# Kernel tuning notes

Measured on AMD Instinct MI355X. Metric: run time of the kernel, lower is better.

Reference implementation:

```python
import jax, jax.numpy as jnp
import numpy as np

N, T, H, D = 8, 192, 1024, 128
P = 4            # t_patch_size (kernel = stride)
TP = T // P      # 48 patch tokens
E = 16384
HOUR, WDAY = 48, 7


def conv1d_patch(e, W, b):
    # e: [B, Cin, T]; W: [Cout, Cin, P]; kernel == stride == P (non-overlapping)
    B, Ci, Tt = e.shape
    e = e.reshape(B, Ci, Tt // P, P)
    return jnp.einsum('bctk,ock->bot', e, W) + b[None, :, None]  # [B, Cout, T']


def gcn_propagate(x, src, dst, coef):
    # x: [B, H, D] ; symmetric-normalized sparse A_hat @ x
    msg = x[:, src, :] * coef[None, :, None]
    return jnp.zeros_like(x).at[:, dst, :].add(msg)


def setup_inputs() -> dict:
    key = jax.random.key(0)
    ks = jax.random.split(key, 12)
    x = jax.random.normal(ks[0], (N, 1, T, H, 1), dtype=jnp.float32)
    x_mark = jax.random.randint(ks[1], (N, T, 2), 0, 7).astype(jnp.int64)
    edges = jax.random.randint(ks[2], (E, 2), 0, H).astype(jnp.int64)
    node_split = jnp.arange(H, dtype=jnp.int64).reshape(4, 256)
    s = 0.02
    params = {
        'hour_emb': jax.random.normal(ks[3], (HOUR, D), jnp.float32) * s,
        'weekday_emb': jax.random.normal(ks[4], (WDAY, D), jnp.float32) * s,
        'timeconv_w': jax.random.normal(ks[5], (D, D, P), jnp.float32) * s,
        'timeconv_b': jnp.zeros((D,), jnp.float32),
        'tconv_w': jax.random.normal(ks[6], (D, 1, P), jnp.float32) * s,
        'tconv_b': jnp.zeros((D,), jnp.float32),
        'W1': jax.random.normal(ks[7], (D, D), jnp.float32) * s,
        'b1': jnp.zeros((D,), jnp.float32),
        'W2': jax.random.normal(ks[8], (D, D), jnp.float32) * s,
        'b2': jnp.zeros((D,), jnp.float32),
    }
    return dict(x=x, x_mark=x_mark, edges=edges, node_split=node_split, **params)


def reference(x, x_mark, edges, node_split, hour_emb, weekday_emb,
              timeconv_w, timeconv_b, tconv_w, tconv_b, W1, b1, W2, b2):
    # ---- TimeEmb (TemporalEmbedding, hour_num='48') ----
    hour_x = hour_emb[x_mark[:, :, 1]]        # [N, T, D]
    wday_x = weekday_emb[x_mark[:, :, 0]]     # [N, T, D]
    time_emb = conv1d_patch((hour_x + wday_x).transpose(0, 2, 1),
                            timeconv_w, timeconv_b).transpose(0, 2, 1)  # [N, T', D]

    # ---- temporal value embedding ----
    xv = jnp.squeeze(x, (1, 4)).transpose(0, 2, 1).reshape(N * H, 1, T)  # [N*H,1,T]
    tv = conv1d_patch(xv, tconv_w, tconv_b)                 # [N*H, D, T']
    tv = tv.transpose(0, 2, 1).reshape(N, H, TP, D)         # [N, H, T', D]
    tv = tv.transpose(0, 2, 1, 3).reshape(N * TP, H, D)     # [N*T', H, D]

    # ---- 2-layer GCN with self-loops + symmetric normalization ----
    src = jnp.concatenate([edges[:, 0], jnp.arange(H)])
    dst = jnp.concatenate([edges[:, 1], jnp.arange(H)])
    deg = jnp.zeros((H,), tv.dtype).at[dst].add(1.0)
    coef = jax.lax.rsqrt(deg[src] * deg[dst])
    h = jax.nn.relu(gcn_propagate(tv, src, dst, coef) @ W1 + b1)
    token = gcn_propagate(h, src, dst, coef) @ W2 + b2      # [N*T', H, D]
    token = token.reshape(N, TP, H, D)

    # ---- per-group gather + mean pooling, interleaved per time step ----
    G = node_split.shape[0]
    grouped = token[:, :, node_split.reshape(-1), :].reshape(N, TP, G, -1, D)
    token = grouped.mean(axis=3).reshape(N, TP * G, D)      # [N, T'*G, D]

    time_rep = jnp.repeat(time_emb, G, axis=1)              # [N, T'*G, D]
    out = token + time_rep  # is_time == 1; eval mode -> no dropout
    return out, time_rep
```

## Files before the change

### kernel.cpp

```cpp
#include <hip/hip_runtime.h>
#include <hip/hip_bf16.h>

#define NN 8
#define TT 192
#define HH 1024
#define DD 128
#define TPP 48
#define EE 16384
#define NEDGE (EE + HH)
#define BB (NN * TPP)
#define NOUT (NN * TT * DD)

typedef short bf16x8 __attribute__((ext_vector_type(8)));
typedef float f32x4 __attribute__((ext_vector_type(4)));

__device__ __forceinline__ float bf2f(__hip_bfloat16 h) { return __bfloat162float(h); }
__device__ __forceinline__ float us2f(unsigned short u) {
  union { unsigned i; float f; } t;
  t.i = ((unsigned)u) << 16;
  return t.f;
}

__global__ __launch_bounds__(256) void k_setup(
    const int* __restrict__ edges, int* __restrict__ degE,
    const int* __restrict__ node_split, int* __restrict__ inv,
    const float* __restrict__ tw, float* __restrict__ twT,
    float* __restrict__ zbuf,
    const float* __restrict__ x, __hip_bfloat16* __restrict__ Xall) {
  __shared__ float tile[64][65];
  int tid = threadIdx.x, bid = blockIdx.x;
  int i = bid * 256 + tid;
  if (i < EE) atomicAdd(&degE[edges[2 * i + 1]], 1);
  if (i < HH) inv[node_split[i]] = i;
  if (i < 65536) twT[(i & 511) * DD + (i >> 9)] = tw[i];
  if (i < 6144) zbuf[i] = 0.f;

  int tt = bid % 24, st = bid / 24;
  int t0 = tt * 64, s0 = st * 64;
  int sl = tid & 63, r4 = tid >> 6;
#pragma unroll 4
  for (int ii = 0; ii < 16; ++ii) {
    int tl = ii * 4 + r4;
    tile[tl][sl] = x[(size_t)(t0 + tl) * HH + s0 + sl];
  }
  __syncthreads();
#pragma unroll 4
  for (int ii = 0; ii < 16; ++ii) {
    int sl2 = ii * 4 + r4;
    Xall[(size_t)(s0 + sl2) * 1536 + t0 + sl] = __float2bfloat16(tile[sl][sl2]);
  }
}

__global__ __launch_bounds__(1024) void k_scan(const int* __restrict__ degE,
                                               int* __restrict__ row_ptr,
                                               const float* __restrict__ tcw,
                                               const float* __restrict__ tcb,
                                               const float* __restrict__ W1,
                                               float* __restrict__ CW,
                                               const float* __restrict__ W2,
                                               __hip_bfloat16* __restrict__ w2sw) {
  int t = threadIdx.x, lane = t & 63, wid = t >> 6;
  int v = degE[t] + 1;
#pragma unroll
  for (int off = 1; off < 64; off <<= 1) {
    int u = __shfl_up(v, off, 64);
    if (lane >= off) v += u;
  }
  __shared__ int wsum[16];
  if (lane == 63) wsum[wid] = v;
  __syncthreads();
  if (t < 64) {
    int s = (lane < 16) ? wsum[lane] : 0;
#pragma unroll
    for (int off = 1; off < 16; off <<= 1) {
      int u = __shfl_up(s, off, 64);
      if (lane >= off) s += u;
    }
    if (lane < 16) wsum[lane] = s;
  }
  __syncthreads();
  int base = wid ? wsum[wid - 1] : 0;
  row_ptr[t + 1] = base + v;
  if (t == 0) row_ptr[0] = 0;

  if (t < 640) {
    int j = t >> 7, o = t & 127;
    float acc = 0.f;
    if (j < 4)
      for (int d = 0; d < DD; ++d) acc = fmaf(tcw[d * 4 + j], W1[d * DD + o], acc);
    else
      for (int d = 0; d < DD; ++d) acc = fmaf(tcb[d], W1[d * DD + o], acc);
    CW[j * DD + o] = acc;
  }
#pragma unroll 4
  for (int u = 0; u < 16; ++u) {
    int i = t * 16 + u;
    int n = i >> 7, k = i & 127;
    int dstb = n * 256 + (((k >> 3) ^ (n & 7)) * 16) + (k & 7) * 2;
    w2sw[dstb >> 1] = __float2bfloat16(W2[k * DD + n]);
  }
}

__global__ void k_scatter(const int* __restrict__ edges, const int* __restrict__ degE,
                          const int* __restrict__ row_ptr, const int* __restrict__ inv,
                          int* __restrict__ fill, int* __restrict__ csr_src,
                          float* __restrict__ csr_coef, float* __restrict__ csum,
                          float* __restrict__ QT) {
  int e = blockIdx.x * 256 + threadIdx.x;
  if (e >= NEDGE) return;
  int s, dt;
  if (e < EE) { s = edges[2 * e]; dt = edges[2 * e + 1]; }
  else        { s = dt = e - EE; }
  float ds = (float)(degE[s] + 1);
  float dd = (float)(degE[dt] + 1);
  float cf = rsqrtf(ds * dd);
  int pos = atomicAdd(&fill[dt], 1);
  int at = row_ptr[dt] + pos;
  csr_src[at] = s;
  csr_coef[at] = cf;
  atomicAdd(&csum[dt], cf);
  int g = inv[dt] >> 8;
  atomicAdd(&QT[s * 4 + g], cf * (1.0f / 256.0f));
}

__global__ __launch_bounds__(256) void k_spmm(
    const int* __restrict__ row_ptr, const int* __restrict__ csr_src,
    const float* __restrict__ csr_coef, const __hip_bfloat16* __restrict__ Xall,
    __hip_bfloat16* __restrict__ xbar,
    const int* __restrict__ xm, const float* __restrict__ hour_emb,
    const float* __restrict__ wday_emb, const float* __restrict__ twT,
    const float* __restrict__ tcb, float* __restrict__ out) {
  __shared__ float sL[2][512];
  int tid = threadIdx.x, bid = blockIdx.x;
  if (bid < HH) {
    int h = bid;
    int j0 = row_ptr[h], j1 = row_ptr[h + 1];
    float a0 = 0.f, a1 = 0.f, a2 = 0.f, a3 = 0.f, a4 = 0.f, a5 = 0.f;
    for (int j = j0; j < j1; ++j) {
      int s = csr_src[j];
      float cf = csr_coef[j];
      const unsigned* xr = (const unsigned*)(Xall + (size_t)s * 1536);
      unsigned u0 = xr[tid], u1 = xr[tid + 256], u2 = xr[tid + 512];
      union { unsigned i; float f; } lo, hi;
      lo.i = u0 << 16; hi.i = u0 & 0xffff0000u;
      a0 = fmaf(cf, lo.f, a0); a1 = fmaf(cf, hi.f, a1);
      lo.i = u1 << 16; hi.i = u1 & 0xffff0000u;
      a2 = fmaf(cf, lo.f, a2); a3 = fmaf(cf, hi.f, a3);
      lo.i = u2 << 16; hi.i = u2 & 0xffff0000u;
      a4 = fmaf(cf, lo.f, a4); a5 = fmaf(cf, hi.f, a5);
    }
    unsigned* xw = (unsigned*)(xbar + (size_t)h * 1536);
    union { __hip_bfloat16 h2[2]; unsigned u; } pk;
    pk.h2[0] = __float2bfloat16(a0); pk.h2[1] = __float2bfloat16(a1);
    xw[tid] = pk.u;
    pk.h2[0] = __float2bfloat16(a2); pk.h2[1] = __float2bfloat16(a3);
    xw[tid + 256] = pk.u;
    pk.h2[0] = __float2bfloat16(a4); pk.h2[1] = __float2bfloat16(a5);
    xw[tid + 512] = pk.u;
  } else {
    int bb = bid - HH;
    int half = tid >> 7, o = tid & 127;
    int b = bb * 2 + half;
    int n = b / TPP, tp = b % TPP;
    for (int k = 0; k < 4; ++k) {
      int t = tp * 4 + k;
      int wd = xm[(n * TT + t) * 2 + 0];
      int hr = xm[(n * TT + t) * 2 + 1];
      sL[half][o * 4 + k] = hour_emb[hr * DD + o] + wday_emb[wd * DD + o];
    }
    __syncthreads();
    float a0 = tcb[o], a1 = 0.f, a2 = 0.f, a3 = 0.f;
    for (int j = 0; j < 512; j += 4) {
      a0 = fmaf(sL[half][j + 0], twT[(j + 0) * DD + o], a0);
      a1 = fmaf(sL[half][j + 1], twT[(j + 1) * DD + o], a1);
      a2 = fmaf(sL[half][j + 2], twT[(j + 2) * DD + o], a2);
      a3 = fmaf(sL[half][j + 3], twT[(j + 3) * DD + o], a3);
    }
    float acc = (a0 + a1) + (a2 + a3);
    size_t base = (size_t)NOUT + ((size_t)n * TT + tp * 4) * DD + o;
    out[base] = acc;
    out[base + DD] = acc;
    out[base + 2 * DD] = acc;
    out[base + 3 * DD] = acc;
  }
}

__global__ __launch_bounds__(256) void k_red(const __hip_bfloat16* __restrict__ xbar,
                                             const float* __restrict__ csum,
                                             const float* __restrict__ QT,
                                             const float* __restrict__ CW,
                                             const float* __restrict__ b1,
                                             float* __restrict__ ypar) {
  __shared__ float4 xb4[256];
  __shared__ float4 qv[256];
  __shared__ float csv[256];
  __shared__ float yL[512];
  int tid = threadIdx.x, bid = blockIdx.x;
  int b = bid >> 2, qt = bid & 3;
  int h = qt * 256 + tid;
  {
    ushort4 us = *(const ushort4*)(xbar + (size_t)h * 1536 + b * 4);
    xb4[tid] = make_float4(us2f(us.x), us2f(us.y), us2f(us.z), us2f(us.w));
    qv[tid] = *(const float4*)(QT + h * 4);
    csv[tid] = csum[h];
  }
  int o = tid & 127, sub = tid >> 7;
  float cw0 = CW[o], cw1 = CW[DD + o], cw2 = CW[2 * DD + o];
  float cw3 = CW[3 * DD + o], cw4 = CW[4 * DD + o];
  float b1o = b1[o];
  __syncthreads();
  float y0 = 0.f, y1 = 0.f, y2 = 0.f, y3 = 0.f;
  int hh0 = sub * 128;
#pragma unroll 4
  for (int hh = hh0; hh < hh0 + 128; ++hh) {
    float4 xv = xb4[hh];
    float4 q = qv[hh];
    float c = csv[hh];
    float t = fmaf(c, cw4, b1o);
    t = fmaf(xv.x, cw0, t);
    t = fmaf(xv.y, cw1, t);
    t = fmaf(xv.z, cw2, t);
    t = fmaf(xv.w, cw3, t);
    t = fmaxf(t, 0.f);
    y0 = fmaf(q.x, t, y0);
    y1 = fmaf(q.y, t, y1);
    y2 = fmaf(q.z, t, y2);
    y3 = fmaf(q.w, t, y3);
  }
  if (sub == 0) {
    yL[o] = y0; yL[DD + o] = y1; yL[2 * DD + o] = y2; yL[3 * DD + o] = y3;
  }
  __syncthreads();
  if (sub == 1) {
    yL[o] += y0; yL[DD + o] += y1; yL[2 * DD + o] += y2; yL[3 * DD + o] += y3;
  }
  __syncthreads();
  float* yp = ypar + ((size_t)qt * BB + b) * 512;
  yp[tid] = yL[tid];
  yp[tid + 256] = yL[tid + 256];
}

__global__ __launch_bounds__(256, 2) void k_out(const float* __restrict__ ypar,
                                                const __hip_bfloat16* __restrict__ w2sw,
                                                const float* __restrict__ b2,
                                                float* __restrict__ out) {
  __shared__ __align__(16) char Wr[32768];
  __shared__ __align__(16) char Gr[16384];
  int tid = threadIdx.x;
  int m0 = blockIdx.x * 64;
  {
    const uint4* ws = (const uint4*)w2sw;
    uint4* wd = (uint4*)Wr;
    for (int i = tid; i < 2048; i += 256) wd[i] = ws[i];
  }
#pragma unroll 4
  for (int it = 0; it < 16; ++it) {
    int pi = it * 256 + tid;
    int row = pi >> 6, kp = pi & 63;
    int base = (m0 + row) * 128 + 2 * kp;
    float s0 = 0.f, s1 = 0.f;
#pragma unroll
    for (int p = 0; p < 4; ++p) {
      s0 += ypar[(size_t)p * (BB * 512) + base];
      s1 += ypar[(size_t)p * (BB * 512) + base + 1];
    }
    union { __hip_bfloat16 h[2]; unsigned u; } pk;
    pk.h[0] = __float2bfloat16(s0);
    pk.h[1] = __float2bfloat16(s1);
    *(unsigned*)(Gr + row * 256 + (((kp >> 2) ^ (row & 7)) * 16) + (kp & 3) * 4) = pk.u;
  }
  int lane = tid & 63, w = tid >> 6;
  int colq = lane & 15, quad = lane >> 4;
  float bo[8];
#pragma unroll
  for (int jn = 0; jn < 8; ++jn) bo[jn] = b2[jn * 16 + colq];
  __syncthreads();

  f32x4 acc[8];
#pragma unroll
  for (int jn = 0; jn < 8; ++jn) acc[jn] = (f32x4){0.f, 0.f, 0.f, 0.f};
  int arow = w * 16 + colq;
#pragma unroll
  for (int kc = 0; kc < 4; ++kc) {
    bf16x8 af = *(const bf16x8*)(Gr + arow * 256 + (((kc * 4 + quad) ^ (arow & 7)) * 16));
#pragma unroll
    for (int jn = 0; jn < 8; ++jn) {
      int nr = jn * 16 + colq;
      bf16x8 bf = *(const bf16x8*)(Wr + nr * 256 + (((kc * 4 + quad) ^ (nr & 7)) * 16));
      acc[jn] = __builtin_amdgcn_mfma_f32_16x16x32_bf16(af, bf, acc[jn], 0, 0, 0);
    }
  }
#pragma unroll
  for (int reg = 0; reg < 4; ++reg) {
    int m = m0 + w * 16 + quad * 4 + reg;
    int b = m >> 2, g = m & 3;
    int n_ = b / TPP, tp = b % TPP;
    size_t rb = ((size_t)(n_ * TT + tp * 4 + g)) * DD;
#pragma unroll
    for (int jn = 0; jn < 8; ++jn) {
      int o = jn * 16 + colq;
      out[rb + o] = acc[jn][reg] + bo[jn] + out[(size_t)NOUT + rb + o];
    }
  }
}

extern "C" void kernel_launch(void* const* d_in, const int* in_sizes, int n_in,
                              void* d_out, int out_size, void* d_ws, size_t ws_size,
                              hipStream_t stream) {
  const float* x = (const float*)d_in[0];
  const int* xm = (const int*)d_in[1];
  const int* edges = (const int*)d_in[2];
  const int* node_split = (const int*)d_in[3];
  const float* hour_emb = (const float*)d_in[4];
  const float* wday_emb = (const float*)d_in[5];
  const float* timeconv_w = (const float*)d_in[6];
  const float* timeconv_b = (const float*)d_in[7];
  const float* tcw = (const float*)d_in[8];
  const float* tcb = (const float*)d_in[9];
  const float* W1 = (const float*)d_in[10];
  const float* b1 = (const float*)d_in[11];
  const float* W2 = (const float*)d_in[12];
  const float* b2 = (const float*)d_in[13];
  float* out = (float*)d_out;

  char* w = (char*)d_ws;
  int* degE = (int*)(w + 0);
  int* fill = (int*)(w + 4096);
  float* csum = (float*)(w + 8192);
  float* QT = (float*)(w + 12288);
  int* row_ptr = (int*)(w + 28672);
  int* inv = (int*)(w + 33024);
  int* csr_src = (int*)(w + 37120);
  float* csr_coef = (float*)(w + 106752);
  __hip_bfloat16* w2sw = (__hip_bfloat16*)(w + 176384);
  float* CW = (float*)(w + 209152);
  float* twT = (float*)(w + 213248);
  __hip_bfloat16* Xall = (__hip_bfloat16*)(w + 475392);
  float* ypar = (float*)(w + 475392);
  __hip_bfloat16* xbar = (__hip_bfloat16*)(w + 3621120);

  hipMemsetAsync(degE, 0, 4096, stream);
  k_setup<<<384, 256, 0, stream>>>(edges, degE, node_split, inv, timeconv_w, twT,
                                   (float*)(w + 4096), x, Xall);
  k_scan<<<1, 1024, 0, stream>>>(degE, row_ptr, tcw, tcb, W1, CW, W2, w2sw);
  k_scatter<<<68, 256, 0, stream>>>(edges, degE, row_ptr, inv, fill, csr_src, csr_coef,
                                    csum, QT);
  k_spmm<<<HH + BB / 2, 256, 0, stream>>>(row_ptr, csr_src, csr_coef, Xall, xbar, xm,
                                          hour_emb, wday_emb, twT, timeconv_b, out);
  k_red<<<BB * 4, 256, 0, stream>>>(xbar, csum, QT, CW, b1, ypar);
  k_out<<<24, 256, 0, stream>>>(ypar, w2sw, b2, out);
}
```

Measured before the change: 156.5 us.

## Eliminate scan kernel, fold weight prep into setup, unroll SpMM gathers

The single-block scan kernel is removed. Its CW and W2-swizzle work moves into extra blocks of the setup kernel, and every scatter block now recomputes the degree prefix sum in shared memory, so one launch and a serial 1-block stage are gone. The SpMM stages neighbor indices and coefficients in LDS and unrolls the gather by four to keep more loads in flight. k_red is reshaped to 128 threads, each computing two output columns. The cost is redundant scan work in each of the 68 scatter blocks, plus more registers in k_red.

New measurement: 143.7 us. 1.09x faster.

```diff
diff --git a/kernel.cpp b/kernel.cpp
--- a/kernel.cpp
+++ b/kernel.cpp
@@ -14,11 +14,22 @@
 typedef short bf16x8 __attribute__((ext_vector_type(8)));
 typedef float f32x4 __attribute__((ext_vector_type(4)));
 
-__device__ __forceinline__ float bf2f(__hip_bfloat16 h) { return __bfloat162float(h); }
 __device__ __forceinline__ float us2f(unsigned short u) {
   union { unsigned i; float f; } t;
   t.i = ((unsigned)u) << 16;
   return t.f;
+}
+
+__device__ __forceinline__ void acc6(float cf, unsigned u0, unsigned u1, unsigned u2,
+                                     float& a0, float& a1, float& a2, float& a3,
+                                     float& a4, float& a5) {
+  union { unsigned i; float f; } lo, hi;
+  lo.i = u0 << 16; hi.i = u0 & 0xffff0000u;
+  a0 = fmaf(cf, lo.f, a0); a1 = fmaf(cf, hi.f, a1);
+  lo.i = u1 << 16; hi.i = u1 & 0xffff0000u;
+  a2 = fmaf(cf, lo.f, a2); a3 = fmaf(cf, hi.f, a3);
+  lo.i = u2 << 16; hi.i = u2 & 0xffff0000u;
+  a4 = fmaf(cf, lo.f, a4); a5 = fmaf(cf, hi.f, a5);
 }
 
 __global__ __launch_bounds__(256) void k_setup(
@@ -26,101 +37,102 @@
     const int* __restrict__ node_split, int* __restrict__ inv,
     const float* __restrict__ tw, float* __restrict__ twT,
     float* __restrict__ zbuf,
-    const float* __restrict__ x, __hip_bfloat16* __restrict__ Xall) {
+    const float* __restrict__ x, __hip_bfloat16* __restrict__ Xall,
+    const float* __restrict__ tcw, const float* __restrict__ tcb,
+    const float* __restrict__ W1, float* __restrict__ CW,
+    const float* __restrict__ W2, __hip_bfloat16* __restrict__ w2sw) {
   __shared__ float tile[64][65];
   int tid = threadIdx.x, bid = blockIdx.x;
-  int i = bid * 256 + tid;
-  if (i < EE) atomicAdd(&degE[edges[2 * i + 1]], 1);
-  if (i < HH) inv[node_split[i]] = i;
-  if (i < 65536) twT[(i & 511) * DD + (i >> 9)] = tw[i];
-  if (i < 6144) zbuf[i] = 0.f;
-
-  int tt = bid % 24, st = bid / 24;
-  int t0 = tt * 64, s0 = st * 64;
-  int sl = tid & 63, r4 = tid >> 6;
+  if (bid < 384) {
+    int i = bid * 256 + tid;
+    if (i < EE) atomicAdd(&degE[edges[2 * i + 1]], 1);
+    if (i < HH) inv[node_split[i]] = i;
+    if (i < 65536) twT[(i & 511) * DD + (i >> 9)] = tw[i];
+    if (i < 6144) zbuf[i] = 0.f;
+
+    int tt = bid % 24, st = bid / 24;
+    int t0 = tt * 64, s0 = st * 64;
+    int sl = tid & 63, r4 = tid >> 6;
 #pragma unroll 4
-  for (int ii = 0; ii < 16; ++ii) {
-    int tl = ii * 4 + r4;
-    tile[tl][sl] = x[(size_t)(t0 + tl) * HH + s0 + sl];
-  }
-  __syncthreads();
+    for (int ii = 0; ii < 16; ++ii) {
+      int tl = ii * 4 + r4;
+      tile[tl][sl] = x[(size_t)(t0 + tl) * HH + s0 + sl];
+    }
+    __syncthreads();
 #pragma unroll 4
-  for (int ii = 0; ii < 16; ++ii) {
-    int sl2 = ii * 4 + r4;
-    Xall[(size_t)(s0 + sl2) * 1536 + t0 + sl] = __float2bfloat16(tile[sl][sl2]);
-  }
-}
-
-__global__ __launch_bounds__(1024) void k_scan(const int* __restrict__ degE,
-                                               int* __restrict__ row_ptr,
-                                               const float* __restrict__ tcw,
-                                               const float* __restrict__ tcb,
-                                               const float* __restrict__ W1,
-                                               float* __restrict__ CW,
-                                               const float* __restrict__ W2,
-                                               __hip_bfloat16* __restrict__ w2sw) {
-  int t = threadIdx.x, lane = t & 63, wid = t >> 6;
-  int v = degE[t] + 1;
+    for (int ii = 0; ii < 16; ++ii) {
+      int sl2 = ii * 4 + r4;
+      Xall[(size_t)(s0 + sl2) * 1536 + t0 + sl] = __float2bfloat16(tile[sl][sl2]);
+    }
+  } else {
+    int ex = (bid - 384) * 256 + tid;
+    if (ex < 640) {
+      int j = ex >> 7, o = ex & 127;
+      float acc = 0.f;
+      if (j < 4)
+        for (int d = 0; d < DD; ++d) acc = fmaf(tcw[d * 4 + j], W1[d * DD + o], acc);
+      else
+        for (int d = 0; d < DD; ++d) acc = fmaf(tcb[d], W1[d * DD + o], acc);
+      CW[j * DD + o] = acc;
+    }
+    int ew = ex - 1024;
+    if (ew >= 0 && ew < 16384) {
+      int n = ew >> 7, k = ew & 127;
+      int dstb = n * 256 + (((k >> 3) ^ (n & 7)) * 16) + (k & 7) * 2;
+      w2sw[dstb >> 1] = __float2bfloat16(W2[k * DD + n]);
+    }
+  }
+}
+
+__global__ __launch_bounds__(256) void k_scatter(
+    const int* __restrict__ edges, const int* __restrict__ degE,
+    const int* __restrict__ inv, int* __restrict__ fill,
+    int* __restrict__ csr_src, float* __restrict__ csr_coef,
+    float* __restrict__ csum, float* __restrict__ QT, int* __restrict__ row_ptr) {
+  __shared__ int rp[1024];
+  __shared__ int wsumS[4];
+  int tid = threadIdx.x, lane = tid & 63, wid = tid >> 6;
+  int4 d4 = ((const int4*)degE)[tid];
+  int l0 = d4.x + 1, l1 = d4.y + 1, l2 = d4.z + 1, l3 = d4.w + 1;
+  int lsum = l0 + l1 + l2 + l3;
+  int incl = lsum;
 #pragma unroll
   for (int off = 1; off < 64; off <<= 1) {
-    int u = __shfl_up(v, off, 64);
-    if (lane >= off) v += u;
-  }
-  __shared__ int wsum[16];
-  if (lane == 63) wsum[wid] = v;
-  __syncthreads();
-  if (t < 64) {
-    int s = (lane < 16) ? wsum[lane] : 0;
-#pragma unroll
-    for (int off = 1; off < 16; off <<= 1) {
-      int u = __shfl_up(s, off, 64);
-      if (lane >= off) s += u;
-    }
-    if (lane < 16) wsum[lane] = s;
-  }
-  __syncthreads();
-  int base = wid ? wsum[wid - 1] : 0;
-  row_ptr[t + 1] = base + v;
-  if (t == 0) row_ptr[0] = 0;
-
-  if (t < 640) {
-    int j = t >> 7, o = t & 127;
-    float acc = 0.f;
-    if (j < 4)
-      for (int d = 0; d < DD; ++d) acc = fmaf(tcw[d * 4 + j], W1[d * DD + o], acc);
-    else
-      for (int d = 0; d < DD; ++d) acc = fmaf(tcb[d], W1[d * DD + o], acc);
-    CW[j * DD + o] = acc;
-  }
-#pragma unroll 4
-  for (int u = 0; u < 16; ++u) {
-    int i = t * 16 + u;
-    int n = i >> 7, k = i & 127;
-    int dstb = n * 256 + (((k >> 3) ^ (n & 7)) * 16) + (k & 7) * 2;
-    w2sw[dstb >> 1] = __float2bfloat16(W2[k * DD + n]);
-  }
-}
-
-__global__ void k_scatter(const int* __restrict__ edges, const int* __restrict__ degE,
-                          const int* __restrict__ row_ptr, const int* __restrict__ inv,
-                          int* __restrict__ fill, int* __restrict__ csr_src,
-                          float* __restrict__ csr_coef, float* __restrict__ csum,
-                          float* __restrict__ QT) {
-  int e = blockIdx.x * 256 + threadIdx.x;
-  if (e >= NEDGE) return;
-  int s, dt;
-  if (e < EE) { s = edges[2 * e]; dt = edges[2 * e + 1]; }
-  else        { s = dt = e - EE; }
-  float ds = (float)(degE[s] + 1);
-  float dd = (float)(degE[dt] + 1);
-  float cf = rsqrtf(ds * dd);
-  int pos = atomicAdd(&fill[dt], 1);
-  int at = row_ptr[dt] + pos;
-  csr_src[at] = s;
-  csr_coef[at] = cf;
-  atomicAdd(&csum[dt], cf);
-  int g = inv[dt] >> 8;
-  atomicAdd(&QT[s * 4 + g], cf * (1.0f / 256.0f));
+    int u = __shfl_up(incl, off, 64);
+    if (lane >= off) incl += u;
+  }
+  if (lane == 63) wsumS[wid] = incl;
+  __syncthreads();
+  int base = 0;
+  if (wid > 0) base += wsumS[0];
+  if (wid > 1) base += wsumS[1];
+  if (wid > 2) base += wsumS[2];
+  int excl = base + incl - lsum;
+  rp[4 * tid] = excl;
+  rp[4 * tid + 1] = excl + l0;
+  rp[4 * tid + 2] = excl + l0 + l1;
+  rp[4 * tid + 3] = excl + l0 + l1 + l2;
+  __syncthreads();
+  if (blockIdx.x == 0) {
+    for (int i = tid; i < 1024; i += 256) row_ptr[i] = rp[i];
+    if (tid == 0) row_ptr[1024] = NEDGE;
+  }
+  int e = blockIdx.x * 256 + tid;
+  if (e < NEDGE) {
+    int s, dt;
+    if (e < EE) { s = edges[2 * e]; dt = edges[2 * e + 1]; }
+    else        { s = dt = e - EE; }
+    float ds = (float)(degE[s] + 1);
+    float dd = (float)(degE[dt] + 1);
+    float cf = rsqrtf(ds * dd);
+    int pos = atomicAdd(&fill[dt], 1);
+    int at = rp[dt] + pos;
+    csr_src[at] = s;
+    csr_coef[at] = cf;
+    atomicAdd(&csum[dt], cf);
+    int g = inv[dt] >> 8;
+    atomicAdd(&QT[s * 4 + g], cf * (1.0f / 256.0f));
+  }
 }
 
 __global__ __launch_bounds__(256) void k_spmm(
@@ -131,23 +143,44 @@
     const float* __restrict__ wday_emb, const float* __restrict__ twT,
     const float* __restrict__ tcb, float* __restrict__ out) {
   __shared__ float sL[2][512];
+  __shared__ int sS[256];
+  __shared__ float sC[256];
   int tid = threadIdx.x, bid = blockIdx.x;
   if (bid < HH) {
     int h = bid;
     int j0 = row_ptr[h], j1 = row_ptr[h + 1];
+    int cnt = j1 - j0;
+    int cs = cnt < 256 ? cnt : 256;
+    if (tid < cs) { sS[tid] = csr_src[j0 + tid]; sC[tid] = csr_coef[j0 + tid]; }
+    __syncthreads();
     float a0 = 0.f, a1 = 0.f, a2 = 0.f, a3 = 0.f, a4 = 0.f, a5 = 0.f;
-    for (int j = j0; j < j1; ++j) {
-      int s = csr_src[j];
-      float cf = csr_coef[j];
+    int j = 0;
+    for (; j + 4 <= cs; j += 4) {
+      const unsigned* x0 = (const unsigned*)(Xall + (size_t)sS[j] * 1536);
+      const unsigned* x1 = (const unsigned*)(Xall + (size_t)sS[j + 1] * 1536);
+      const unsigned* x2 = (const unsigned*)(Xall + (size_t)sS[j + 2] * 1536);
+      const unsigned* x3 = (const unsigned*)(Xall + (size_t)sS[j + 3] * 1536);
+      unsigned u00 = x0[tid], u01 = x0[tid + 256], u02 = x0[tid + 512];
+      unsigned u10 = x1[tid], u11 = x1[tid + 256], u12 = x1[tid + 512];
+      unsigned u20 = x2[tid], u21 = x2[tid + 256], u22 = x2[tid + 512];
+      unsigned u30 = x3[tid], u31 = x3[tid + 256], u32 = x3[tid + 512];
+      float c0 = sC[j], c1 = sC[j + 1], c2 = sC[j + 2], c3 = sC[j + 3];
+      acc6(c0, u00, u01, u02, a0, a1, a2, a3, a4, a5);
+      acc6(c1, u10, u11, u12, a0, a1, a2, a3, a4, a5);
+      acc6(c2, u20, u21, u22, a0, a1, a2, a3, a4, a5);
+      acc6(c3, u30, u31, u32, a0, a1, a2, a3, a4, a5);
+    }
+    for (; j < cs; ++j) {
+      const unsigned* xr = (const unsigned*)(Xall + (size_t)sS[j] * 1536);
+      unsigned u0 = xr[tid], u1 = xr[tid + 256], u2 = xr[tid + 512];
+      acc6(sC[j], u0, u1, u2, a0, a1, a2, a3, a4, a5);
+    }
+    for (; j < cnt; ++j) {
+      int s = csr_src[j0 + j];
+      float cf = csr_coef[j0 + j];
       const unsigned* xr = (const unsigned*)(Xall + (size_t)s * 1536);
       unsigned u0 = xr[tid], u1 = xr[tid + 256], u2 = xr[tid + 512];
-      union { unsigned i; float f; } lo, hi;
-      lo.i = u0 << 16; hi.i = u0 & 0xffff0000u;
-      a0 = fmaf(cf, lo.f, a0); a1 = fmaf(cf, hi.f, a1);
-      lo.i = u1 << 16; hi.i = u1 & 0xffff0000u;
-      a2 = fmaf(cf, lo.f, a2); a3 = fmaf(cf, hi.f, a3);
-      lo.i = u2 << 16; hi.i = u2 & 0xffff0000u;
-      a4 = fmaf(cf, lo.f, a4); a5 = fmaf(cf, hi.f, a5);
+      acc6(cf, u0, u1, u2, a0, a1, a2, a3, a4, a5);
     }
     unsigned* xw = (unsigned*)(xbar + (size_t)h * 1536);
     union { __hip_bfloat16 h2[2]; unsigned u; } pk;
@@ -185,7 +218,7 @@
   }
 }
 
-__global__ __launch_bounds__(256) void k_red(const __hip_bfloat16* __restrict__ xbar,
+__global__ __launch_bounds__(128) void k_red(const __hip_bfloat16* __restrict__ xbar,
                                              const float* __restrict__ csum,
                                              const float* __restrict__ QT,
                                              const float* __restrict__ CW,
@@ -197,47 +230,58 @@
   __shared__ float yL[512];
   int tid = threadIdx.x, bid = blockIdx.x;
   int b = bid >> 2, qt = bid & 3;
-  int h = qt * 256 + tid;
-  {
+  for (int r = tid; r < 256; r += 128) {
+    int h = qt * 256 + r;
     ushort4 us = *(const ushort4*)(xbar + (size_t)h * 1536 + b * 4);
-    xb4[tid] = make_float4(us2f(us.x), us2f(us.y), us2f(us.z), us2f(us.w));
-    qv[tid] = *(const float4*)(QT + h * 4);
-    csv[tid] = csum[h];
-  }
-  int o = tid & 127, sub = tid >> 7;
-  float cw0 = CW[o], cw1 = CW[DD + o], cw2 = CW[2 * DD + o];
-  float cw3 = CW[3 * DD + o], cw4 = CW[4 * DD + o];
-  float b1o = b1[o];
-  __syncthreads();
-  float y0 = 0.f, y1 = 0.f, y2 = 0.f, y3 = 0.f;
-  int hh0 = sub * 128;
+    xb4[r] = make_float4(us2f(us.x), us2f(us.y), us2f(us.z), us2f(us.w));
+    qv[r] = *(const float4*)(QT + h * 4);
+    csv[r] = csum[h];
+  }
+  int lane = tid & 63, w = tid >> 6;
+  int o0 = lane, o1 = lane + 64;
+  float cw0a = CW[o0], cw1a = CW[DD + o0], cw2a = CW[2 * DD + o0];
+  float cw3a = CW[3 * DD + o0], cw4a = CW[4 * DD + o0];
+  float cw0b = CW[o1], cw1b = CW[DD + o1], cw2b = CW[2 * DD + o1];
+  float cw3b = CW[3 * DD + o1], cw4b = CW[4 * DD + o1];
+  float b1a = b1[o0], b1b = b1[o1];
+  __syncthreads();
+  float y0a = 0.f, y1a = 0.f, y2a = 0.f, y3a = 0.f;
+  float y0b = 0.f, y1b = 0.f, y2b = 0.f, y3b = 0.f;
+  int h0 = w * 128;
 #pragma unroll 4
-  for (int hh = hh0; hh < hh0 + 128; ++hh) {
+  for (int hh = h0; hh < h0 + 128; ++hh) {
     float4 xv = xb4[hh];
     float4 q = qv[hh];
     float c = csv[hh];
-    float t = fmaf(c, cw4, b1o);
-    t = fmaf(xv.x, cw0, t);
-    t = fmaf(xv.y, cw1, t);
-    t = fmaf(xv.z, cw2, t);
-    t = fmaf(xv.w, cw3, t);
-    t = fmaxf(t, 0.f);
-    y0 = fmaf(q.x, t, y0);
-    y1 = fmaf(q.y, t, y1);
-    y2 = fmaf(q.z, t, y2);
-    y3 = fmaf(q.w, t, y3);
-  }
-  if (sub == 0) {
-    yL[o] = y0; yL[DD + o] = y1; yL[2 * DD + o] = y2; yL[3 * DD + o] = y3;
-  }
-  __syncthreads();
-  if (sub == 1) {
-    yL[o] += y0; yL[DD + o] += y1; yL[2 * DD + o] += y2; yL[3 * DD + o] += y3;
+    float t0 = fmaf(c, cw4a, b1a);
+    t0 = fmaf(xv.x, cw0a, t0);
+    t0 = fmaf(xv.y, cw1a, t0);
+    t0 = fmaf(xv.z, cw2a, t0);
+    t0 = fmaf(xv.w, cw3a, t0);
+    t0 = fmaxf(t0, 0.f);
+    float t1 = fmaf(c, cw4b, b1b);
+    t1 = fmaf(xv.x, cw0b, t1);
+    t1 = fmaf(xv.y, cw1b, t1);
+    t1 = fmaf(xv.z, cw2b, t1);
+    t1 = fmaf(xv.w, cw3b, t1);
+    t1 = fmaxf(t1, 0.f);
+    y0a = fmaf(q.x, t0, y0a); y1a = fmaf(q.y, t0, y1a);
+    y2a = fmaf(q.z, t0, y2a); y3a = fmaf(q.w, t0, y3a);
+    y0b = fmaf(q.x, t1, y0b); y1b = fmaf(q.y, t1, y1b);
+    y2b = fmaf(q.z, t1, y2b); y3b = fmaf(q.w, t1, y3b);
+  }
+  if (w == 0) {
+    yL[o0] = y0a; yL[128 + o0] = y1a; yL[256 + o0] = y2a; yL[384 + o0] = y3a;
+    yL[o1] = y0b; yL[128 + o1] = y1b; yL[256 + o1] = y2b; yL[384 + o1] = y3b;
+  }
+  __syncthreads();
+  if (w == 1) {
+    yL[o0] += y0a; yL[128 + o0] += y1a; yL[256 + o0] += y2a; yL[384 + o0] += y3a;
+    yL[o1] += y0b; yL[128 + o1] += y1b; yL[256 + o1] += y2b; yL[384 + o1] += y3b;
   }
   __syncthreads();
   float* yp = ypar + ((size_t)qt * BB + b) * 512;
-  yp[tid] = yL[tid];
-  yp[tid + 256] = yL[tid + 256];
+  for (int i = tid; i < 512; i += 128) yp[i] = yL[i];
 }
 
 __global__ __launch_bounds__(256, 2) void k_out(const float* __restrict__ ypar,
@@ -340,13 +384,13 @@
   __hip_bfloat16* xbar = (__hip_bfloat16*)(w + 3621120);
 
   hipMemsetAsync(degE, 0, 4096, stream);
-  k_setup<<<384, 256, 0, stream>>>(edges, degE, node_split, inv, timeconv_w, twT,
-                                   (float*)(w + 4096), x, Xall);
-  k_scan<<<1, 1024, 0, stream>>>(degE, row_ptr, tcw, tcb, W1, CW, W2, w2sw);
-  k_scatter<<<68, 256, 0, stream>>>(edges, degE, row_ptr, inv, fill, csr_src, csr_coef,
-                                    csum, QT);
+  k_setup<<<452, 256, 0, stream>>>(edges, degE, node_split, inv, timeconv_w, twT,
+                                   (float*)(w + 4096), x, Xall, tcw, tcb, W1, CW, W2,
+                                   w2sw);
+  k_scatter<<<68, 256, 0, stream>>>(edges, degE, inv, fill, csr_src, csr_coef, csum,
+                                    QT, row_ptr);
   k_spmm<<<HH + BB / 2, 256, 0, stream>>>(row_ptr, csr_src, csr_coef, Xall, xbar, xm,
                                           hour_emb, wday_emb, twT, timeconv_b, out);
-  k_red<<<BB * 4, 256, 0, stream>>>(xbar, csum, QT, CW, b1, ypar);
+  k_red<<<BB * 4, 128, 0, stream>>>(xbar, csum, QT, CW, b1, ypar);
   k_out<<<24, 256, 0, stream>>>(ypar, w2sw, b2, out);
 }
```
